# Kernel tuning notes

Measured on AMD Instinct MI355X. Metric: run time of the kernel, lower is better.

## Reference

```python
import jax, jax.numpy as jnp
import numpy as np

EMBED_DIM = 1024
NUM_HEADS = 16
HEAD_DIM = EMBED_DIM // NUM_HEADS
NEG_INF = -1e9


def setup_inputs() -> dict:
    key = jax.random.key(0)
    k1, k2, k3, k4, k5 = jax.random.split(key, 5)
    # ragged batch: 8 segments, alternating lengths 1024 / 512 -> 6144 tokens
    lengths = np.array([1024, 512, 1024, 512, 1024, 512, 1024, 512], dtype=np.int32)
    cu_seqlens = np.concatenate([[0], np.cumsum(lengths)]).astype(np.int32)
    total = int(cu_seqlens[-1])  # 6144
    scale = 0.02
    return {
        "hidden_states": jax.random.normal(k1, (total, EMBED_DIM), dtype=jnp.float32),
        "proj_weight": jax.random.normal(k2, (3 * EMBED_DIM, EMBED_DIM), dtype=jnp.float32) * scale,
        "proj_bias": jax.random.normal(k3, (3 * EMBED_DIM,), dtype=jnp.float32) * scale,
        "out_weight": jax.random.normal(k4, (EMBED_DIM, EMBED_DIM), dtype=jnp.float32) * scale,
        "out_bias": jax.random.normal(k5, (EMBED_DIM,), dtype=jnp.float32) * scale,
        "cu_seqlens": jnp.asarray(cu_seqlens),
        "max_len": 1024,
    }


def reference(hidden_states, proj_weight, proj_bias, out_weight, out_bias, cu_seqlens, max_len):
    T = hidden_states.shape[0]
    B = cu_seqlens.shape[0] - 1
    H, Dh = NUM_HEADS, HEAD_DIM
    softmax_scale = 1.0 / jnp.sqrt(jnp.float32(Dh))

    # fused QKV projection: [T, 3E] -> [T, H, 3, Dh]
    qkv = hidden_states @ proj_weight.T + proj_bias
    qkv = qkv.reshape(T, H, 3, Dh)
    q, k, v = qkv[:, :, 0], qkv[:, :, 1], qkv[:, :, 2]  # each [T, H, Dh]

    # unpack ragged tokens into padded [B, S, H, Dh]
    lengths = cu_seqlens[1:] - cu_seqlens[:-1]            # [B]
    pos = jnp.arange(max_len)                              # [S]
    valid = pos[None, :] < lengths[:, None]                # [B, S]
    idx = jnp.where(valid, cu_seqlens[:-1, None] + pos[None, :], 0)  # [B, S]
    qp, kp, vp = q[idx], k[idx], v[idx]                    # [B, S, H, Dh]

    # per-segment attention (non-causal encoder self-attn)
    scores = jnp.einsum("bqhd,bkhd->bhqk", qp, kp) * softmax_scale  # [B,H,S,S]
    scores = jnp.where(valid[:, None, None, :], scores, NEG_INF)
    probs = jax.nn.softmax(scores, axis=-1)
    ctx = jnp.einsum("bhqk,bkhd->bqhd", probs, vp)         # [B, S, H, Dh]

    # pack back to ragged [T, E]; invalid slots scattered out-of-bounds (dropped)
    scatter_idx = jnp.where(valid, idx, T).reshape(-1)     # [B*S]
    ctx_flat = ctx.reshape(B * max_len, H * Dh)
    context = jnp.zeros((T, H * Dh), dtype=ctx_flat.dtype).at[scatter_idx].set(
        ctx_flat, mode="drop")

    return context @ out_weight.T + out_bias
```

## Files before the change

### kernel.cpp

```cpp
#include <hip/hip_runtime.h>
#include <math.h>

#define EMBED 1024
#define NHEAD 16
#define HDIM 64
#define QKV_LD 3072
#define SM_SCALE_LOG2 0.18033688f

typedef _Float16 f16x8 __attribute__((ext_vector_type(8)));
typedef float f32x4 __attribute__((ext_vector_type(4)));
typedef unsigned short ushort8v __attribute__((ext_vector_type(8)));
typedef unsigned short ushort4v __attribute__((ext_vector_type(4)));

__device__ __forceinline__ void gload16(const void* g, void* l) {
    __builtin_amdgcn_global_load_lds(
        (const __attribute__((address_space(1))) unsigned int*)g,
        (__attribute__((address_space(3))) unsigned int*)l, 16, 0, 0);
}

__device__ __forceinline__ int xcd_swz(int bid, int nwg) {
    int cpx = nwg >> 3;
    return (bid & 7) * cpx + (bid >> 3);
}

__device__ __forceinline__ int swz(int row, int col) {
    return row * 72 + (col ^ (((row >> 3) & 7) << 3));
}

__global__ __launch_bounds__(256) void cvt_f32_f16(
    const float* __restrict__ x, _Float16* __restrict__ y, int n4)
{
    int i = blockIdx.x * 256 + threadIdx.x;
    if (i >= n4) return;
    float4 v = reinterpret_cast<const float4*>(x)[i];
    unsigned short h0 = __builtin_bit_cast(unsigned short, (_Float16)v.x);
    unsigned short h1 = __builtin_bit_cast(unsigned short, (_Float16)v.y);
    unsigned short h2 = __builtin_bit_cast(unsigned short, (_Float16)v.z);
    unsigned short h3 = __builtin_bit_cast(unsigned short, (_Float16)v.w);
    reinterpret_cast<ushort4*>(y)[i] = make_ushort4(h0, h1, h2, h3);
}

template <bool F16_OUT>
__global__ __launch_bounds__(256) void gemm_m97(
    const _Float16* __restrict__ A, const _Float16* __restrict__ B,
    const float* __restrict__ bias, float* __restrict__ Cf,
    _Float16* __restrict__ Ch, int M, int N, int K, int gx)
{
    __shared__ __align__(16) unsigned short sA[128 * 64];
    __shared__ __align__(16) unsigned short sB[128 * 64];

    const int nwg = gridDim.x;
    const int wgid = xcd_swz(blockIdx.x, nwg);
    const int row0 = (wgid / gx) * 128;
    const int col0 = (wgid % gx) * 128;

    const int tid = threadIdx.x;
    const int lane = tid & 63;
    const int w = tid >> 6;
    const int wr = w >> 1;
    const int wc = w & 1;
    const int c = lane & 15;
    const int g = lane >> 4;

    const unsigned short* Au = (const unsigned short*)A;
    const unsigned short* Bu = (const unsigned short*)B;

    f32x4 acc[4][4];
    #pragma unroll
    for (int m = 0; m < 4; m++)
        #pragma unroll
        for (int n = 0; n < 4; n++)
            acc[m][n] = (f32x4){0.f, 0.f, 0.f, 0.f};

    size_t aoff[4], boff[4];
    int ldst[4];
    #pragma unroll
    for (int i = 0; i < 4; i++) {
        int chunk = (i * 4 + w) * 64 + lane;
        int row = chunk >> 3;
        int scol = ((chunk & 7) ^ (row & 7)) * 8;
        aoff[i] = (size_t)min(row0 + row, M - 1) * K + scol;
        boff[i] = (size_t)min(col0 + row, N - 1) * K + scol;
        ldst[i] = chunk * 8;
    }

    for (int k0 = 0; k0 < K; k0 += 64) {
        __syncthreads();
        #pragma unroll
        for (int i = 0; i < 4; i++) {
            gload16(Au + aoff[i] + k0, &sA[ldst[i]]);
            gload16(Bu + boff[i] + k0, &sB[ldst[i]]);
        }
        __syncthreads();

        #pragma unroll
        for (int ks = 0; ks < 2; ks++) {
            f16x8 af[4], bf[4];
            #pragma unroll
            for (int m = 0; m < 4; m++) {
                int row = wr * 64 + m * 16 + c;
                int cc = (ks * 4 + g) ^ (row & 7);
                af[m] = __builtin_bit_cast(f16x8, *reinterpret_cast<const ushort8v*>(
                            &sA[row * 64 + cc * 8]));
            }
            #pragma unroll
            for (int n = 0; n < 4; n++) {
                int row = wc * 64 + n * 16 + c;
                int cc = (ks * 4 + g) ^ (row & 7);
                bf[n] = __builtin_bit_cast(f16x8, *reinterpret_cast<const ushort8v*>(
                            &sB[row * 64 + cc * 8]));
            }
            #pragma unroll
            for (int m = 0; m < 4; m++)
                #pragma unroll
                for (int n = 0; n < 4; n++)
                    acc[m][n] = __builtin_amdgcn_mfma_f32_16x16x32_f16(af[m], bf[n], acc[m][n], 0, 0, 0);
        }
    }

    #pragma unroll
    for (int m = 0; m < 4; m++) {
        #pragma unroll
        for (int n = 0; n < 4; n++) {
            int cc = col0 + wc * 64 + n * 16 + c;
            if (cc >= N) continue;
            float bv = bias[cc];
            #pragma unroll
            for (int j = 0; j < 4; j++) {
                int r = row0 + wr * 64 + m * 16 + g * 4 + j;
                if (r >= M) continue;
                float v = acc[m][n][j] + bv;
                if constexpr (F16_OUT) {
                    Ch[(size_t)r * N + cc] = (_Float16)v;
                } else {
                    Cf[(size_t)r * N + cc] = v;
                }
            }
        }
    }
}

__global__ __launch_bounds__(256) void transpose_v(
    const _Float16* __restrict__ qkv, _Float16* __restrict__ vT, int T, int TP)
{
    __shared__ __align__(16) unsigned short s[64 * 72];
    const int nt = TP >> 6;
    const int h = blockIdx.x / nt;
    const int tt = blockIdx.x % nt;
    const int tid = threadIdx.x;
    const unsigned short* qu = (const unsigned short*)qkv;
    unsigned short* vu = (unsigned short*)vT;

    #pragma unroll
    for (int it = 0; it < 2; it++) {
        int idx = it * 256 + tid;
        int tl = idx >> 3;
        int d0 = (idx & 7) * 8;
        int t = tt * 64 + tl;
        uint4 val = make_uint4(0u, 0u, 0u, 0u);
        if (t < T)
            val = *reinterpret_cast<const uint4*>(&qu[(size_t)t * QKV_LD + h * 192 + 128 + d0]);
        *reinterpret_cast<uint4*>(&s[swz(tl, d0)]) = val;
    }
    __syncthreads();
    #pragma unroll
    for (int it = 0; it < 2; it++) {
        int idx = it * 256 + tid;
        int d = idx >> 3;
        int t0 = (idx & 7) * 8;
        ushort8v o;
        #pragma unroll
        for (int j = 0; j < 8; j++)
            o[j] = s[swz(t0 + j, d)];
        *reinterpret_cast<ushort8v*>(&vu[((size_t)h * 64 + d) * TP + tt * 64 + t0]) = o;
    }
}

__global__ __launch_bounds__(256) void attn_mfma(
    const _Float16* __restrict__ qkv, const _Float16* __restrict__ vT,
    const int* __restrict__ cu, _Float16* __restrict__ ctx,
    int B, int maxTiles, int TP)
{
    __shared__ __align__(16) unsigned short sK[64 * 72];
    __shared__ __align__(16) unsigned short sV[64 * 72];
    __shared__ __align__(16) unsigned short sP[64 * 72];

    const int nwg = gridDim.x;
    const int wgid = xcd_swz(blockIdx.x, nwg);
    const int h = wgid / maxTiles;
    const int tile = wgid % maxTiles;

    int b = -1, q0 = 0, accum = 0;
    for (int i = 0; i < B; i++) {
        int len = cu[i + 1] - cu[i];
        int nt = (len + 63) >> 6;
        if (tile < accum + nt) { b = i; q0 = (tile - accum) << 6; break; }
        accum += nt;
    }
    if (b < 0) return;
    const int s0 = cu[b];
    const int L = cu[b + 1] - s0;
    if (q0 >= L) return;

    const int tid = threadIdx.x;
    const int lane = tid & 63;
    const int w = tid >> 6;
    const int g = lane >> 4;
    const int c = lane & 15;
    const size_t qcol = (size_t)h * 192;
    const unsigned short* qkvu = (const unsigned short*)qkv;
    const unsigned short* vTu = (const unsigned short*)vT;

    f16x8 q[2];
    {
        int qrow = min(q0 + w * 16 + c, L - 1);
        size_t off = (size_t)(s0 + qrow) * QKV_LD + qcol + g * 8;
        q[0] = *reinterpret_cast<const f16x8*>(&qkv[off]);
        q[1] = *reinterpret_cast<const f16x8*>(&qkv[off + 32]);
    }

    const int r_ = tid >> 3;
    const int d0_ = (tid & 7) * 8;
    const int lst0 = swz(r_, d0_);
    const int lst1 = swz(32 + r_, d0_);
    const size_t kband = qcol + 64 + d0_;
    const size_t vband0 = ((size_t)h * 64 + r_) * TP + s0 + d0_;
    const size_t vband1 = vband0 + (size_t)32 * TP;

    uint4 pk0, pk1, pv0, pv1;
    {
        int gr0 = min(r_, L - 1);
        int gr1 = min(32 + r_, L - 1);
        pk0 = *reinterpret_cast<const uint4*>(&qkvu[(size_t)(s0 + gr0) * QKV_LD + kband]);
        pk1 = *reinterpret_cast<const uint4*>(&qkvu[(size_t)(s0 + gr1) * QKV_LD + kband]);
        pv0 = *reinterpret_cast<const uint4*>(&vTu[vband0]);
        pv1 = *reinterpret_cast<const uint4*>(&vTu[vband1]);
    }

    f32x4 o[4];
    #pragma unroll
    for (int n = 0; n < 4; n++) o[n] = (f32x4){0.f, 0.f, 0.f, 0.f};
    float m_r = -INFINITY;
    float l_r = 0.f;

    for (int kc = 0; kc < L; kc += 64) {
        __syncthreads();
        *reinterpret_cast<uint4*>(&sK[lst0]) = pk0;
        *reinterpret_cast<uint4*>(&sK[lst1]) = pk1;
        *reinterpret_cast<uint4*>(&sV[lst0]) = pv0;
        *reinterpret_cast<uint4*>(&sV[lst1]) = pv1;
        __syncthreads();

        if (kc + 64 < L) {
            int nkc = kc + 64;
            int gr0 = min(nkc + r_, L - 1);
            int gr1 = min(nkc + 32 + r_, L - 1);
            pk0 = *reinterpret_cast<const uint4*>(&qkvu[(size_t)(s0 + gr0) * QKV_LD + kband]);
            pk1 = *reinterpret_cast<const uint4*>(&qkvu[(size_t)(s0 + gr1) * QKV_LD + kband]);
            pv0 = *reinterpret_cast<const uint4*>(&vTu[vband0 + nkc]);
            pv1 = *reinterpret_cast<const uint4*>(&vTu[vband1 + nkc]);
        }

        __builtin_amdgcn_s_setprio(1);
        f32x4 sacc[4];
        #pragma unroll
        for (int f = 0; f < 4; f++) sacc[f] = (f32x4){0.f, 0.f, 0.f, 0.f};
        #pragma unroll
        for (int f = 0; f < 4; f++) {
            #pragma unroll
            for (int ks = 0; ks < 2; ks++) {
                f16x8 kf = __builtin_bit_cast(f16x8, *reinterpret_cast<const ushort8v*>(
                               &sK[swz(f * 16 + c, ks * 32 + g * 8)]));
                sacc[f] = __builtin_amdgcn_mfma_f32_16x16x32_f16(kf, q[ks], sacc[f], 0, 0, 0);
            }
        }
        __builtin_amdgcn_s_setprio(0);

        float mx = -INFINITY;
        if (kc + 64 <= L) {
            #pragma unroll
            for (int f = 0; f < 4; f++) {
                #pragma unroll
                for (int j = 0; j < 4; j++) {
                    float v = sacc[f][j] * SM_SCALE_LOG2;
                    sacc[f][j] = v;
                    mx = fmaxf(mx, v);
                }
            }
        } else {
            #pragma unroll
            for (int f = 0; f < 4; f++) {
                #pragma unroll
                for (int j = 0; j < 4; j++) {
                    float v = sacc[f][j] * SM_SCALE_LOG2;
                    if (kc + f * 16 + g * 4 + j >= L) v = -1.0e9f;
                    sacc[f][j] = v;
                    mx = fmaxf(mx, v);
                }
            }
        }
        mx = fmaxf(mx, __shfl_xor(mx, 16));
        mx = fmaxf(mx, __shfl_xor(mx, 32));
        float mn = fmaxf(m_r, mx);
        float fs = exp2f(m_r - mn);
        float rs = 0.f;
        #pragma unroll
        for (int f = 0; f < 4; f++) {
            unsigned short hv[4];
            #pragma unroll
            for (int j = 0; j < 4; j++) {
                float p = exp2f(sacc[f][j] - mn);
                rs += p;
                hv[j] = __builtin_bit_cast(unsigned short, (_Float16)p);
            }
            *reinterpret_cast<ushort4v*>(&sP[swz(w * 16 + c, f * 16 + g * 4)]) =
                (ushort4v){hv[0], hv[1], hv[2], hv[3]};
        }
        rs += __shfl_xor(rs, 16);
        rs += __shfl_xor(rs, 32);
        l_r = l_r * fs + rs;
        m_r = mn;

        #pragma unroll
        for (int j = 0; j < 4; j++) {
            float fq = __shfl(fs, (lane & 48) | (g * 4 + j));
            #pragma unroll
            for (int n = 0; n < 4; n++)
                o[n][j] *= fq;
        }

        f16x8 pa[2];
        #pragma unroll
        for (int ks = 0; ks < 2; ks++)
            pa[ks] = __builtin_bit_cast(f16x8, *reinterpret_cast<const ushort8v*>(
                         &sP[swz(w * 16 + c, ks * 32 + g * 8)]));
        __builtin_amdgcn_s_setprio(1);
        #pragma unroll
        for (int n = 0; n < 4; n++) {
            #pragma unroll
            for (int ks = 0; ks < 2; ks++) {
                f16x8 vf = __builtin_bit_cast(f16x8, *reinterpret_cast<const ushort8v*>(
                               &sV[swz(n * 16 + c, ks * 32 + g * 8)]));
                o[n] = __builtin_amdgcn_mfma_f32_16x16x32_f16(pa[ks], vf, o[n], 0, 0, 0);
            }
        }
        __builtin_amdgcn_s_setprio(0);
    }

    float linv[4];
    {
        float il = 1.0f / l_r;
        #pragma unroll
        for (int j = 0; j < 4; j++)
            linv[j] = __shfl(il, (lane & 48) | (g * 4 + j));
    }
    #pragma unroll
    for (int n = 0; n < 4; n++) {
        #pragma unroll
        for (int j = 0; j < 4; j++) {
            int r = q0 + w * 16 + g * 4 + j;
            if (r >= L) continue;
            ctx[(size_t)(s0 + r) * EMBED + h * HDIM + n * 16 + c] =
                (_Float16)(o[n][j] * linv[j]);
        }
    }
}

extern "C" void kernel_launch(void* const* d_in, const int* in_sizes, int n_in,
                              void* d_out, int out_size, void* d_ws, size_t ws_size,
                              hipStream_t stream) {
    const float* hs = (const float*)d_in[0];
    const float* pw = (const float*)d_in[1];
    const float* pb = (const float*)d_in[2];
    const float* ow = (const float*)d_in[3];
    const float* ob = (const float*)d_in[4];
    const int*   cu = (const int*)d_in[5];

    const int T = in_sizes[0] / EMBED;
    const int B = in_sizes[5] - 1;
    const int TP = ((T + 63) & ~63) + 64;

    char* p = (char*)d_ws;
    size_t hsF_b  = (size_t)T * EMBED * sizeof(_Float16);
    size_t pwF_b  = (size_t)3 * EMBED * EMBED * sizeof(_Float16);
    size_t owF_b  = (size_t)EMBED * EMBED * sizeof(_Float16);
    size_t qkvF_b = (size_t)T * QKV_LD * sizeof(_Float16);
    size_t ctxF_b = hsF_b;
    size_t vT_b   = (size_t)NHEAD * 64 * TP * sizeof(_Float16);

    _Float16* hsF  = (_Float16*)p;  p += hsF_b;
    _Float16* pwF  = (_Float16*)p;  p += pwF_b;
    _Float16* owF  = (_Float16*)p;  p += owF_b;
    _Float16* qkvF = (_Float16*)p;  p += qkvF_b;
    _Float16* ctxF = (_Float16*)p;  p += ctxF_b;
    _Float16* vTF  = (_Float16*)p;  p += vT_b;

    float* out = (float*)d_out;
    dim3 blk(256);

    {
        int n4 = T * EMBED / 4;
        cvt_f32_f16<<<(n4 + 255) / 256, blk, 0, stream>>>(hs, hsF, n4);
        n4 = 3 * EMBED * EMBED / 4;
        cvt_f32_f16<<<(n4 + 255) / 256, blk, 0, stream>>>(pw, pwF, n4);
        n4 = EMBED * EMBED / 4;
        cvt_f32_f16<<<(n4 + 255) / 256, blk, 0, stream>>>(ow, owF, n4);
    }

    {
        int gx = (3 * EMBED) / 128;
        int nwg = gx * ((T + 127) / 128);
        gemm_m97<true><<<nwg, blk, 0, stream>>>(hsF, pwF, pb,
                                                (float*)nullptr, qkvF,
                                                T, 3 * EMBED, EMBED, gx);
    }

    {
        int nwg = NHEAD * (TP / 64);
        transpose_v<<<nwg, blk, 0, stream>>>(qkvF, vTF, T, TP);
    }

    {
        int maxTiles = T / 64 + B;
        int nwg = NHEAD * maxTiles;
        attn_mfma<<<nwg, blk, 0, stream>>>(qkvF, vTF, cu, ctxF, B, maxTiles, TP);
    }

    {
        int gx = EMBED / 128;
        int nwg = gx * ((T + 127) / 128);
        gemm_m97<false><<<nwg, blk, 0, stream>>>(ctxF, owF, ob,
                                                 out, (_Float16*)nullptr,
                                                 T, EMBED, EMBED, gx);
    }
}
```

Before: 185.7 us.

## Reorder attention tiles longest-first with heads interleaved; skip rescale when max stable

The attention kernel now puts the head index in the fastest-varying part of the workgroup ID. Query tiles are assigned in descending tile-level order across segments, so work is spread over heads and the longer segments' tiles go first. The online softmax also skips rescaling the accumulator and running sum unless some lane's new max exceeds the old one by more than 8 (in log2 units), which removes exp2 and shuffle work in most iterations. The lazy rescale lets probabilities reach up to 2^8 before rescaling, a small fp16 overflow and precision risk, and the new tile mapping adds a nested scan per block.

After: 211.1 us. 1.14x slower.

```diff
diff --git a/kernel.cpp b/kernel.cpp
--- a/kernel.cpp
+++ b/kernel.cpp
@@ -187,20 +187,30 @@
 
     const int nwg = gridDim.x;
     const int wgid = xcd_swz(blockIdx.x, nwg);
-    const int h = wgid / maxTiles;
-    const int tile = wgid % maxTiles;
-
-    int b = -1, q0 = 0, accum = 0;
+    const int h = wgid % NHEAD;
+    const int pairRank = wgid / NHEAD;
+
+    int maxNt = 0;
     for (int i = 0; i < B; i++) {
-        int len = cu[i + 1] - cu[i];
-        int nt = (len + 63) >> 6;
-        if (tile < accum + nt) { b = i; q0 = (tile - accum) << 6; break; }
-        accum += nt;
+        int nt = (cu[i + 1] - cu[i] + 63) >> 6;
+        maxNt = max(maxNt, nt);
+    }
+    int b = -1, q0 = 0;
+    {
+        int rank = pairRank;
+        for (int lvl = maxNt - 1; lvl >= 0 && b < 0; --lvl) {
+            for (int i = 0; i < B; i++) {
+                int nt = (cu[i + 1] - cu[i] + 63) >> 6;
+                if (nt > lvl) {
+                    if (rank == 0) { b = i; q0 = lvl << 6; break; }
+                    --rank;
+                }
+            }
+        }
     }
     if (b < 0) return;
     const int s0 = cu[b];
     const int L = cu[b + 1] - s0;
-    if (q0 >= L) return;
 
     const int tid = threadIdx.x;
     const int lane = tid & 63;
@@ -301,8 +311,10 @@
         }
         mx = fmaxf(mx, __shfl_xor(mx, 16));
         mx = fmaxf(mx, __shfl_xor(mx, 32));
-        float mn = fmaxf(m_r, mx);
-        float fs = exp2f(m_r - mn);
+
+        const bool nskip = !__all(mx - m_r <= 8.0f);
+        const float mn = nskip ? fmaxf(m_r, mx) : m_r;
+
         float rs = 0.f;
         #pragma unroll
         for (int f = 0; f < 4; f++) {
@@ -318,15 +330,20 @@
         }
         rs += __shfl_xor(rs, 16);
         rs += __shfl_xor(rs, 32);
-        l_r = l_r * fs + rs;
-        m_r = mn;
-
-        #pragma unroll
-        for (int j = 0; j < 4; j++) {
-            float fq = __shfl(fs, (lane & 48) | (g * 4 + j));
-            #pragma unroll
-            for (int n = 0; n < 4; n++)
-                o[n][j] *= fq;
+
+        if (nskip) {
+            float fs = exp2f(m_r - mn);
+            l_r = l_r * fs + rs;
+            m_r = mn;
+            #pragma unroll
+            for (int j = 0; j < 4; j++) {
+                float fq = __shfl(fs, (lane & 48) | (g * 4 + j));
+                #pragma unroll
+                for (int n = 0; n < 4; n++)
+                    o[n][j] *= fq;
+            }
+        } else {
+            l_r += rs;
         }
 
         f16x8 pa[2];
```
